# Kernel tuning notes

Measured on AMD Instinct MI355X. Metric: run time of the kernel, lower is better.

## Reference

```python
import jax, jax.numpy as jnp
import numpy as np

EPS = 1e-5

def activation_quant(x):
    # per-token absmax int8 quantization (fake-quant, STE)
    scale = 127.0 / jnp.clip(jnp.max(jnp.abs(x), axis=-1, keepdims=True), EPS, None)
    xq = jnp.clip(jnp.round(x * scale), -128.0, 127.0) / scale
    return x + jax.lax.stop_gradient(xq - x)

def weight_quant(w):
    # per-tensor ternary quantization with mean-abs scale (BitNet b1.58)
    scale = 1.0 / jnp.clip(jnp.mean(jnp.abs(w)), EPS, None)
    wq = jnp.clip(jnp.round(w * scale), -1.0, 1.0) / scale
    return w + jax.lax.stop_gradient(wq - w)

def bitlinear(x, w):
    # w: [out, in]; y = x_q @ w_q^T
    return jnp.einsum('bsd,od->bso', activation_quant(x), weight_quant(w))

def setup_inputs() -> dict:
    key = jax.random.key(0)
    k1, k2, k3 = jax.random.split(key, 3)
    dim, inner = 2048, 8192
    x = jax.random.normal(k1, (4, 2048, dim), dtype=jnp.float32)
    w1 = jax.random.normal(k2, (inner, dim), dtype=jnp.float32) * (dim ** -0.5)
    w2 = jax.random.normal(k3, (dim, inner), dtype=jnp.float32) * (inner ** -0.5)
    return {"x": x, "w1": w1, "w2": w2}

def reference(x, w1, w2):
    h = bitlinear(x, w1)          # [B, S, inner]
    h = jax.nn.relu(h)
    return bitlinear(h, w2)       # [B, S, dim]
```

## Files before the change

kernel.cpp:

```cpp
#include <hip/hip_runtime.h>
#include <hip/hip_bf16.h>
#include <stdint.h>

#define EPSQ 1e-5f

typedef int i32x4 __attribute__((ext_vector_type(4)));

__device__ inline void gload16(const void* g, void* l){
  __builtin_amdgcn_global_load_lds((const __attribute__((address_space(1))) unsigned int*)g,
                                   (__attribute__((address_space(3))) unsigned int*)l, 16, 0, 0);
}

__device__ inline unsigned pack4(float4 v, float s, float lo, float hi){
  int a = (int)fminf(fmaxf(rintf(v.x*s), lo), hi);
  int b = (int)fminf(fmaxf(rintf(v.y*s), lo), hi);
  int c = (int)fminf(fmaxf(rintf(v.z*s), lo), hi);
  int d = (int)fminf(fmaxf(rintf(v.w*s), lo), hi);
  return (unsigned)((a&255)|((b&255)<<8)|((c&255)<<16)|((d&255)<<24));
}

__global__ void absmean2(const float* __restrict__ w1, const float* __restrict__ w2,
                         int n4, double* __restrict__ partial){
  const int half = blockIdx.x >> 10;
  const float4* w4 = (const float4*)(half ? w2 : w1);
  double s = 0.0;
  int idx = (blockIdx.x & 1023)*blockDim.x + threadIdx.x;
  int stride = 1024*blockDim.x;
  for (int i = idx; i < n4; i += stride){
    float4 v = w4[i];
    s += (double)(fabsf(v.x)+fabsf(v.y)+fabsf(v.z)+fabsf(v.w));
  }
  __shared__ double sm[256];
  sm[threadIdx.x] = s; __syncthreads();
  for (int o=128;o>0;o>>=1){ if (threadIdx.x<o) sm[threadIdx.x]+=sm[threadIdx.x+o]; __syncthreads(); }
  if (threadIdx.x==0) partial[blockIdx.x] = sm[0];
}

__global__ void finalize_scales(const double* __restrict__ partial, float* __restrict__ scalebuf, double inv_n){
  __shared__ double sm[256];
  int t = threadIdx.x;
  double s1 = partial[t] + partial[t+256] + partial[t+512] + partial[t+768];
  sm[t]=s1; __syncthreads();
  for(int o=128;o>0;o>>=1){ if(t<o) sm[t]+=sm[t+o]; __syncthreads(); }
  double m1 = sm[0];
  __syncthreads();
  double s2 = partial[1024+t]+partial[1280+t]+partial[1536+t]+partial[1792+t];
  sm[t]=s2; __syncthreads();
  for(int o=128;o>0;o>>=1){ if(t<o) sm[t]+=sm[t+o]; __syncthreads(); }
  if (t==0){
    scalebuf[0] = 1.0f / fmaxf((float)(m1*inv_n),    EPSQ);
    scalebuf[1] = 1.0f / fmaxf((float)(sm[0]*inv_n), EPSQ);
  }
}

__global__ void wquant8(const float* __restrict__ w, char* __restrict__ wq,
                        const float* __restrict__ scalebuf, int which){
  int i = blockIdx.x*256 + threadIdx.x;
  float s = scalebuf[which];
  const float4* w4 = (const float4*)w;
  float4 v0 = w4[(size_t)i*4], v1 = w4[(size_t)i*4+1], v2 = w4[(size_t)i*4+2], v3 = w4[(size_t)i*4+3];
  uint4 pk = make_uint4(pack4(v0,s,-1.f,1.f), pack4(v1,s,-1.f,1.f),
                        pack4(v2,s,-1.f,1.f), pack4(v3,s,-1.f,1.f));
  *reinterpret_cast<uint4*>(wq + (size_t)i*16) = pk;
}

__global__ void aquant8c(const float* __restrict__ x, char* __restrict__ xq,
                         float* __restrict__ s_a, int* __restrict__ rowMax){
  int m = blockIdx.x, t = threadIdx.x;
  if (t==0) rowMax[m] = 0;
  const float4* x4 = (const float4*)(x + (size_t)m*2048);
  float4 a = x4[t*2], b = x4[t*2+1];
  float va[8] = {a.x,a.y,a.z,a.w,b.x,b.y,b.z,b.w};
  float mx = 0.f;
  #pragma unroll
  for (int j=0;j<8;j++) mx = fmaxf(mx, fabsf(va[j]));
  #pragma unroll
  for (int o=1;o<64;o<<=1) mx = fmaxf(mx, __shfl_xor(mx, o, 64));
  __shared__ float wm[4];
  if ((t&63)==0) wm[t>>6] = mx;
  __syncthreads();
  mx = fmaxf(fmaxf(wm[0],wm[1]), fmaxf(wm[2],wm[3]));
  float s = 127.f / fmaxf(mx, EPSQ);
  if (t==0) s_a[m] = s;
  uint2 pk = make_uint2(pack4(a,s,-128.f,127.f), pack4(b,s,-128.f,127.f));
  *reinterpret_cast<uint2*>(xq + (size_t)m*2048 + t*8) = pk;
}

template<int EPI, int STEPS>
__global__ __launch_bounds__(256,2) void gemmK(
    const char* __restrict__ A, const char* __restrict__ B, void* __restrict__ Cv,
    int moff, int* __restrict__ rowMax, const float* __restrict__ s_a,
    const float* __restrict__ scalebuf)
{
  const int Ks = STEPS << 7;
  __shared__ __align__(16) char sm[2*32768 + 1024];
  int* smax = (int*)(sm + 2*32768);
  const int tid = threadIdx.x, lane = tid & 63, w = tid >> 6;
  const int wr = w >> 1, wc = w & 1;
  const int n0 = blockIdx.x*128, m0 = blockIdx.y*128;

  i32x4 acc[4][4] = {};

  const int trow = tid >> 3;
  const int scl  = (tid & 7) ^ (trow & 7);
  const char* gA = A + (size_t)(m0 + trow)*Ks + scl*16;
  const char* gB = B + (size_t)(n0 + trow)*Ks + scl*16;

  auto stage = [&](int sbase, int kt){
    #pragma unroll
    for (int i=0;i<4;i++){
      gload16(gA + kt + (size_t)(i*32)*Ks, sm + sbase + (i*256+tid)*16);
      gload16(gB + kt + (size_t)(i*32)*Ks, sm + sbase + 16384 + (i*256+tid)*16);
    }
  };

  const int frow = lane & 15, kb = lane >> 4;
  int aoff[2][4], boff[2][4];
  #pragma unroll
  for (int kh=0;kh<2;kh++){
    #pragma unroll
    for (int f=0;f<4;f++){
      int ra = wr*64 + f*16 + frow;
      aoff[kh][f] = ra*128 + ((((kh<<2)|kb) ^ (ra&7))<<4);
      int rb = wc*64 + f*16 + frow;
      boff[kh][f] = 16384 + rb*128 + ((((kh<<2)|kb) ^ (rb&7))<<4);
    }
  }

  auto kstep = [&](const int slot, int t, const int mode){
    const char* base = sm + slot*32768;
    i32x4 av0[4], bv0[4], av1[4], bv1[4];
    #pragma unroll
    for (int f=0;f<4;f++){
      av0[f] = *reinterpret_cast<const i32x4*>(base + aoff[0][f]);
      bv0[f] = *reinterpret_cast<const i32x4*>(base + boff[0][f]);
    }
    #pragma unroll
    for (int f=0;f<4;f++){
      av1[f] = *reinterpret_cast<const i32x4*>(base + aoff[1][f]);
      bv1[f] = *reinterpret_cast<const i32x4*>(base + boff[1][f]);
    }
    if (mode == 0) stage((slot^1)*32768, (t+1)<<7);
    asm volatile("s_waitcnt lgkmcnt(8)" ::: "memory");
    __builtin_amdgcn_sched_barrier(0);
    __builtin_amdgcn_s_setprio(1);
    #pragma unroll
    for (int fm=0;fm<4;fm++)
      #pragma unroll
      for (int fn=0;fn<4;fn++)
        acc[fm][fn] = __builtin_amdgcn_mfma_i32_16x16x64_i8(av0[fm], bv0[fn], acc[fm][fn], 0,0,0);
    __builtin_amdgcn_s_setprio(0);
    asm volatile("s_waitcnt lgkmcnt(0)" ::: "memory");
    __builtin_amdgcn_sched_barrier(0);
    __builtin_amdgcn_s_setprio(1);
    #pragma unroll
    for (int fm=0;fm<4;fm++)
      #pragma unroll
      for (int fn=0;fn<4;fn++)
        acc[fm][fn] = __builtin_amdgcn_mfma_i32_16x16x64_i8(av1[fm], bv1[fn], acc[fm][fn], 0,0,0);
    __builtin_amdgcn_s_setprio(0);
    if (mode == 0) asm volatile("s_waitcnt vmcnt(0)" ::: "memory");
    if (mode != 2) __builtin_amdgcn_s_barrier();
  };

  stage(0, 0);
  asm volatile("s_waitcnt vmcnt(0)" ::: "memory");
  __builtin_amdgcn_s_barrier();
  __builtin_amdgcn_sched_barrier(0);

  for (int tt = 0; tt < STEPS/2 - 1; ++tt){
    int t = tt*2;
    kstep(0, t,   0);
    kstep(1, t+1, 0);
  }
  kstep(0, STEPS-2, 0);
  kstep(1, STEPS-1, 2);

  const int cc = lane & 15, cr = (lane >> 4)*4;
  if (EPI == 0){
    __syncthreads();
    if (tid < 128) smax[tid] = 0;
    __syncthreads();
    ushort* C16 = (ushort*)Cv;
    #pragma unroll
    for (int fm=0;fm<4;fm++){
      #pragma unroll
      for (int reg=0;reg<4;reg++){
        int rl = wr*64 + fm*16 + cr + reg;
        size_t r = (size_t)(m0 + rl);
        int rmax = 0;
        #pragma unroll
        for (int fn=0;fn<4;fn++){
          int v = acc[fm][fn][reg]; v = v > 0 ? v : 0;
          C16[r*8192 + n0 + wc*64 + fn*16 + cc] = (ushort)(v > 65535 ? 65535 : v);
          rmax = v > rmax ? v : rmax;
        }
        atomicMax(&smax[rl], rmax);
      }
    }
    __syncthreads();
    if (tid < 128) atomicMax(&rowMax[m0 + tid], smax[tid]);
  } else {
    float* out = (float*)Cv;
    float sw1 = scalebuf[0], sw2 = scalebuf[1];
    #pragma unroll
    for (int fm=0;fm<4;fm++){
      #pragma unroll
      for (int reg=0;reg<4;reg++){
        int rl = wr*64 + fm*16 + cr + reg;
        size_t r = (size_t)(moff + m0 + rl);
        int Mi = rowMax[r];
        float maxref = (float)Mi / (s_a[r]*sw1);
        float inv2 = fmaxf(maxref, EPSQ) / (127.f*sw2);
        #pragma unroll
        for (int fn=0;fn<4;fn++)
          out[r*2048 + n0 + wc*64 + fn*16 + cc] = (float)acc[fm][fn][reg] * inv2;
      }
    }
  }
}

__global__ void hquant(const ushort* __restrict__ h16, char* __restrict__ hq,
                       const int* __restrict__ rowMax){
  int m = blockIdx.y;
  int Mi = rowMax[m];
  float rqv = (Mi > 0) ? 127.f/(float)Mi : 0.f;
  size_t base = (size_t)m*8192 + blockIdx.x*2048 + threadIdx.x*8;
  uint4 pk = *reinterpret_cast<const uint4*>(h16 + base);
  unsigned u[4] = {pk.x, pk.y, pk.z, pk.w};
  unsigned o[2] = {0,0};
  #pragma unroll
  for (int j=0;j<8;j++){
    float h = (float)(u[j>>1] >> ((j&1)*16) & 0xffff);
    int q = (int)fminf(rintf(h*rqv), 127.f);
    o[j>>2] |= (unsigned)(q & 255) << ((j&3)*8);
  }
  *reinterpret_cast<uint2*>(hq + base) = make_uint2(o[0], o[1]);
}

extern "C" void kernel_launch(void* const* d_in, const int* in_sizes, int n_in,
                              void* d_out, int out_size, void* d_ws, size_t ws_size,
                              hipStream_t stream){
  const float* x  = (const float*)d_in[0];
  const float* w1 = (const float*)d_in[1];
  const float* w2 = (const float*)d_in[2];
  float* out = (float*)d_out;

  const int MTOK = 8192, Mc = 1024;
  const size_t nW = (size_t)8192*2048;

  char* ws = (char*)d_ws; size_t off = 0;
  auto alloc = [&](size_t n)->char*{ char* p = ws+off; off = (off+n+255) & ~(size_t)255; return p; };

  float*  s_a     = (float*)alloc((size_t)MTOK*4);
  int*    rowMax  = (int*)  alloc((size_t)MTOK*4);
  float*  scalebuf= (float*)alloc(256);
  double* partial = (double*)alloc(2048*8);
  char*   w1q     = alloc(nW);

  bool sepW2=false, fullA=false; int hqM=4096;
  char *w2q=nullptr, *a8=nullptr, *a8c=nullptr, *hq=nullptr;
  ushort* h16=nullptr;
  if (off + 5*nW + 4096 <= ws_size){
    sepW2 = true; fullA = true;
    w2q = alloc(nW);
    h16 = (ushort*)alloc(nW);
    a8  = alloc(nW);
    hq  = alloc(2*nW);
  } else if (off + 4*nW + 4096 <= ws_size){
    fullA = true;
    h16 = (ushort*)alloc(nW); w2q = (char*)h16;
    a8  = alloc(nW);
    hq  = alloc(2*nW);
  } else {
    h16 = (ushort*)alloc(nW); w2q = (char*)h16;
    a8c = alloc((size_t)Mc*2048);
    hqM = 0;
    for (int m = 4096; m >= 1024; m >>= 1)
      if (off + (size_t)m*8192 <= ws_size){ hqM = m; break; }
    if (!hqM) return;
    hq = alloc((size_t)hqM*8192);
  }

  absmean2<<<2048,256,0,stream>>>(w1, w2, (int)(nW/4), partial);
  finalize_scales<<<1,256,0,stream>>>(partial, scalebuf, 1.0/(double)nW);
  wquant8<<<(int)(nW/16/256),256,0,stream>>>(w1, w1q, scalebuf, 0);
  if (sepW2) wquant8<<<(int)(nW/16/256),256,0,stream>>>(w2, w2q, scalebuf, 1);
  if (fullA) aquant8c<<<MTOK,256,0,stream>>>(x, a8, s_a, rowMax);

  for (int s = 0; s < MTOK/hqM; ++s){
    for (int c = 0; c < hqM/Mc; ++c){
      int ch = s*hqM + c*Mc;
      const char* aptr;
      if (fullA) aptr = a8 + (size_t)ch*2048;
      else {
        aquant8c<<<Mc,256,0,stream>>>(x + (size_t)ch*2048, a8c, s_a + ch, rowMax + ch);
        aptr = a8c;
      }
      gemmK<0,16><<<dim3(64, Mc/128),256,0,stream>>>(
          aptr, w1q, h16, 0, rowMax + ch, nullptr, scalebuf);
      hquant<<<dim3(4, Mc),256,0,stream>>>(h16, hq + (size_t)c*Mc*8192, rowMax + ch);
    }
    if (!sepW2)
      wquant8<<<(int)(nW/16/256),256,0,stream>>>(w2, w2q, scalebuf, 1);
    gemmK<1,64><<<dim3(16, hqM/128),256,0,stream>>>(
        hq, w2q, out, s*hqM, rowMax, s_a, scalebuf);
  }
}
```

Measured before the change: 392.7 us.

## Use two waves per 128x128 GEMM tile, each computing 64x128

The int8 GEMM drops from four waves of 256 threads to two waves of 128 threads per block. Each wave now accumulates a 64x128 sub-tile (4x8 MFMA fragments), so every A fragment read from LDS is reused across twice as many B fragments. Staging loops, epilogues and launch sizes are adjusted to match. This roughly doubles accumulator registers per wave and removes the manual lgkmcnt-split interleaving, which risks lower occupancy and less latency hiding per CU.

```diff
diff --git a/kernel.cpp b/kernel.cpp
--- a/kernel.cpp
+++ b/kernel.cpp
@@ -87,7 +87,7 @@
 }
 
 template<int EPI, int STEPS>
-__global__ __launch_bounds__(256,2) void gemmK(
+__global__ __launch_bounds__(128,1) void gemmK(
     const char* __restrict__ A, const char* __restrict__ B, void* __restrict__ Cv,
     int moff, int* __restrict__ rowMax, const float* __restrict__ s_a,
     const float* __restrict__ scalebuf)
@@ -95,11 +95,11 @@
   const int Ks = STEPS << 7;
   __shared__ __align__(16) char sm[2*32768 + 1024];
   int* smax = (int*)(sm + 2*32768);
-  const int tid = threadIdx.x, lane = tid & 63, w = tid >> 6;
-  const int wr = w >> 1, wc = w & 1;
+  const int tid = threadIdx.x, lane = tid & 63;
+  const int wr = tid >> 6;
   const int n0 = blockIdx.x*128, m0 = blockIdx.y*128;
 
-  i32x4 acc[4][4] = {};
+  i32x4 acc[4][8] = {};
 
   const int trow = tid >> 3;
   const int scl  = (tid & 7) ^ (trow & 7);
@@ -108,57 +108,47 @@
 
   auto stage = [&](int sbase, int kt){
     #pragma unroll
-    for (int i=0;i<4;i++){
-      gload16(gA + kt + (size_t)(i*32)*Ks, sm + sbase + (i*256+tid)*16);
-      gload16(gB + kt + (size_t)(i*32)*Ks, sm + sbase + 16384 + (i*256+tid)*16);
-    }
+    for (int i=0;i<8;i++)
+      gload16(gA + kt + (size_t)(i*16)*Ks, sm + sbase + (i*128+tid)*16);
+    #pragma unroll
+    for (int i=0;i<8;i++)
+      gload16(gB + kt + (size_t)(i*16)*Ks, sm + sbase + 16384 + (i*128+tid)*16);
   };
 
   const int frow = lane & 15, kb = lane >> 4;
-  int aoff[2][4], boff[2][4];
+  int aoff[2][4], boff[2][8];
   #pragma unroll
   for (int kh=0;kh<2;kh++){
     #pragma unroll
     for (int f=0;f<4;f++){
       int ra = wr*64 + f*16 + frow;
       aoff[kh][f] = ra*128 + ((((kh<<2)|kb) ^ (ra&7))<<4);
-      int rb = wc*64 + f*16 + frow;
+    }
+    #pragma unroll
+    for (int f=0;f<8;f++){
+      int rb = f*16 + frow;
       boff[kh][f] = 16384 + rb*128 + ((((kh<<2)|kb) ^ (rb&7))<<4);
     }
   }
 
   auto kstep = [&](const int slot, int t, const int mode){
     const char* base = sm + slot*32768;
-    i32x4 av0[4], bv0[4], av1[4], bv1[4];
-    #pragma unroll
-    for (int f=0;f<4;f++){
-      av0[f] = *reinterpret_cast<const i32x4*>(base + aoff[0][f]);
-      bv0[f] = *reinterpret_cast<const i32x4*>(base + boff[0][f]);
-    }
-    #pragma unroll
-    for (int f=0;f<4;f++){
-      av1[f] = *reinterpret_cast<const i32x4*>(base + aoff[1][f]);
-      bv1[f] = *reinterpret_cast<const i32x4*>(base + boff[1][f]);
-    }
     if (mode == 0) stage((slot^1)*32768, (t+1)<<7);
-    asm volatile("s_waitcnt lgkmcnt(8)" ::: "memory");
-    __builtin_amdgcn_sched_barrier(0);
-    __builtin_amdgcn_s_setprio(1);
-    #pragma unroll
-    for (int fm=0;fm<4;fm++)
-      #pragma unroll
-      for (int fn=0;fn<4;fn++)
-        acc[fm][fn] = __builtin_amdgcn_mfma_i32_16x16x64_i8(av0[fm], bv0[fn], acc[fm][fn], 0,0,0);
-    __builtin_amdgcn_s_setprio(0);
-    asm volatile("s_waitcnt lgkmcnt(0)" ::: "memory");
-    __builtin_amdgcn_sched_barrier(0);
-    __builtin_amdgcn_s_setprio(1);
-    #pragma unroll
-    for (int fm=0;fm<4;fm++)
-      #pragma unroll
-      for (int fn=0;fn<4;fn++)
-        acc[fm][fn] = __builtin_amdgcn_mfma_i32_16x16x64_i8(av1[fm], bv1[fn], acc[fm][fn], 0,0,0);
-    __builtin_amdgcn_s_setprio(0);
+    #pragma unroll
+    for (int kh=0;kh<2;kh++){
+      i32x4 av[4], bv[8];
+      #pragma unroll
+      for (int f=0;f<4;f++) av[f] = *reinterpret_cast<const i32x4*>(base + aoff[kh][f]);
+      #pragma unroll
+      for (int f=0;f<8;f++) bv[f] = *reinterpret_cast<const i32x4*>(base + boff[kh][f]);
+      __builtin_amdgcn_s_setprio(1);
+      #pragma unroll
+      for (int fm=0;fm<4;fm++)
+        #pragma unroll
+        for (int fn=0;fn<8;fn++)
+          acc[fm][fn] = __builtin_amdgcn_mfma_i32_16x16x64_i8(av[fm], bv[fn], acc[fm][fn], 0,0,0);
+      __builtin_amdgcn_s_setprio(0);
+    }
     if (mode == 0) asm volatile("s_waitcnt vmcnt(0)" ::: "memory");
     if (mode != 2) __builtin_amdgcn_s_barrier();
   };
@@ -179,7 +169,7 @@
   const int cc = lane & 15, cr = (lane >> 4)*4;
   if (EPI == 0){
     __syncthreads();
-    if (tid < 128) smax[tid] = 0;
+    smax[tid] = 0;
     __syncthreads();
     ushort* C16 = (ushort*)Cv;
     #pragma unroll
@@ -190,16 +180,16 @@
         size_t r = (size_t)(m0 + rl);
         int rmax = 0;
         #pragma unroll
-        for (int fn=0;fn<4;fn++){
+        for (int fn=0;fn<8;fn++){
           int v = acc[fm][fn][reg]; v = v > 0 ? v : 0;
-          C16[r*8192 + n0 + wc*64 + fn*16 + cc] = (ushort)(v > 65535 ? 65535 : v);
+          C16[r*8192 + n0 + fn*16 + cc] = (ushort)(v > 65535 ? 65535 : v);
           rmax = v > rmax ? v : rmax;
         }
         atomicMax(&smax[rl], rmax);
       }
     }
     __syncthreads();
-    if (tid < 128) atomicMax(&rowMax[m0 + tid], smax[tid]);
+    atomicMax(&rowMax[m0 + tid], smax[tid]);
   } else {
     float* out = (float*)Cv;
     float sw1 = scalebuf[0], sw2 = scalebuf[1];
@@ -213,8 +203,8 @@
         float maxref = (float)Mi / (s_a[r]*sw1);
         float inv2 = fmaxf(maxref, EPSQ) / (127.f*sw2);
         #pragma unroll
-        for (int fn=0;fn<4;fn++)
-          out[r*2048 + n0 + wc*64 + fn*16 + cc] = (float)acc[fm][fn][reg] * inv2;
+        for (int fn=0;fn<8;fn++)
+          out[r*2048 + n0 + fn*16 + cc] = (float)acc[fm][fn][reg] * inv2;
       }
     }
   }
@@ -297,13 +287,13 @@
         aquant8c<<<Mc,256,0,stream>>>(x + (size_t)ch*2048, a8c, s_a + ch, rowMax + ch);
         aptr = a8c;
       }
-      gemmK<0,16><<<dim3(64, Mc/128),256,0,stream>>>(
+      gemmK<0,16><<<dim3(64, Mc/128),128,0,stream>>>(
           aptr, w1q, h16, 0, rowMax + ch, nullptr, scalebuf);
       hquant<<<dim3(4, Mc),256,0,stream>>>(h16, hq + (size_t)c*Mc*8192, rowMax + ch);
     }
     if (!sepW2)
       wquant8<<<(int)(nW/16/256),256,0,stream>>>(w2, w2q, scalebuf, 1);
-    gemmK<1,64><<<dim3(16, hqM/128),256,0,stream>>>(
+    gemmK<1,64><<<dim3(16, hqM/128),128,0,stream>>>(
         hq, w2q, out, s*hqM, rowMax, s_a, scalebuf);
   }
 }
```

Result: slower. 424.6 us (+8.1%).
